# Kernel optimization log

Measured on AMD Instinct MI355X. Metric: run time of the kernel, lower is better.

## Reference

```python
import jax, jax.numpy as jnp
import numpy as np

B, N, D_IN, D_OUT = 4, 1024, 128, 64
SLOPE = 0.01  # LeakyReLU negative slope


def leaky_relu(x):
    return jnp.where(x >= 0, x, SLOPE * x)


def setup_inputs() -> dict:
    key = jax.random.key(0)
    k_x, k_m, k_w1, k_w2, k_a, k_l = jax.random.split(key, 6)
    x = jax.random.normal(k_x, (B, N, D_IN), dtype=jnp.float32)
    # binary adjacency mask; add self-loops so every row has >=1 neighbor
    mask = jax.random.bernoulli(k_m, 0.05, (B, N, N)).astype(jnp.float32)
    eye = jnp.eye(N, dtype=jnp.float32)[None]
    A_shape = jnp.maximum(mask, eye)
    w1 = jax.random.normal(k_w1, (D_IN, D_OUT), dtype=jnp.float32)
    w2 = jax.random.normal(k_w2, (D_IN, D_OUT), dtype=jnp.float32)
    a = jax.random.normal(k_a, (D_OUT,), dtype=jnp.float32)
    lin_w = jax.random.normal(k_l, (D_OUT, D_IN), dtype=jnp.float32) * (1.0 / np.sqrt(D_IN))
    return {"x": x, "A_shape": A_shape, "w1": w1, "w2": w2, "a": a, "lin_w": lin_w}


def reference(x, A_shape, w1, w2, a, lin_w):
    # x: [B,N,D_in], A_shape: [B,N,N] mask
    x1 = x @ w1            # [B,N,D_out]  (dst features)
    x2 = x @ w2            # [B,N,D_out]  (src features)
    # GATv2 additive score: leakyrelu(x1_i + x2_j) . a -> [B,N,N]
    S = leaky_relu(x1[:, :, None, :] + x2[:, None, :, :])
    S = jnp.einsum('bijd,d->bij', S, a)
    S = jnp.tanh(S / 8.0) * 8.0
    A = jnp.exp(S) * A_shape
    A = A / jnp.sum(A, axis=-1, keepdims=True)
    out = A @ x            # [B,N,D_in] weighted aggregate of raw features
    out = out @ lin_w.T    # [B,N,D_out]
    return leaky_relu(out)
```

## Files before the change

### kernel.cpp

```cpp
#include <hip/hip_runtime.h>
#include <math.h>

#define BB 4
#define NN 1024
#define DIN 128
#define DOUT 64
#define SLOPE 0.01f
#define RST 192
#define R1 8


__global__ __launch_bounds__(256, 2) void proj_kernel(
    const float* __restrict__ x, const float* __restrict__ w1,
    const float* __restrict__ w2, const float* __restrict__ lin_w,
    float* __restrict__ x12y) {
  int tid = threadIdx.x;
  int d = tid & 63;
  int g = tid >> 6;
  __shared__ __align__(16) float xl[R1][DIN];
  __shared__ float lwT[DIN][DOUT + 1];
  int row0 = blockIdx.x * R1;

  {
    const float4* xs = reinterpret_cast<const float4*>(x + (size_t)row0 * DIN);
    reinterpret_cast<float4*>(&xl[0][0])[tid] = xs[tid];
  }
#pragma unroll
  for (int i = 0; i < 32; ++i) {
    int idx = i * 256 + tid;
    lwT[idx & 127][idx >> 7] = lin_w[idx];
  }
  __syncthreads();

  float a1[2] = {0.f, 0.f};
  float a2[2] = {0.f, 0.f};
  float a3[2] = {0.f, 0.f};
  const float* w1c = w1 + d;
  const float* w2c = w2 + d;
#pragma unroll 4
  for (int k = 0; k < DIN; ++k) {
    float wv1 = w1c[k * DOUT];
    float wv2 = w2c[k * DOUT];
    float wv3 = lwT[k][d];
#pragma unroll
    for (int r = 0; r < 2; ++r) {
      float xv = xl[g * 2 + r][k];
      a1[r] = fmaf(xv, wv1, a1[r]);
      a2[r] = fmaf(xv, wv2, a2[r]);
      a3[r] = fmaf(xv, wv3, a3[r]);
    }
  }
#pragma unroll
  for (int r = 0; r < 2; ++r) {
    size_t o = (size_t)(row0 + g * 2 + r) * RST;
    x12y[o + d] = a1[r];
    x12y[o + DOUT + d] = a2[r];
    x12y[o + 2 * DOUT + d] = a3[r];
  }
}

__device__ __forceinline__ float fast_edge_exp(float sc) {
  float z = sc * 0.125f;
  z = fminf(10.f, fmaxf(-10.f, z));
  float u = __expf(2.f * z);
  float th = (u - 1.f) / (u + 1.f);
  return __expf(8.f * th);
}

__global__ __launch_bounds__(128, 8) void gat_row_kernel(
    const float* __restrict__ A_shape, const float* __restrict__ a_vec,
    const float* __restrict__ x12y, float* __restrict__ out) {
  int bi = blockIdx.x;
  int b = bi >> 10;
  int tid = threadIdx.x;
  int lane = tid & 63;
  int w = tid >> 6;

  __shared__ int eidx[1040];
  __shared__ __align__(16) float x1s[DOUT];
  __shared__ __align__(16) float avs[DOUT];
  __shared__ float aggh[2][DOUT];
  __shared__ float wsum[2];
  __shared__ int cnt[2];

  if (tid < DOUT) {
    x1s[tid] = x12y[(size_t)bi * RST + tid];
    avs[tid] = a_vec[tid];
  }

  const float* mask_row = A_shape + (size_t)bi * NN + w * 512;
  float mv[8];
#pragma unroll
  for (int c = 0; c < 8; ++c) mv[c] = mask_row[c * 64 + lane];
  int base = 0;
  int seg = w * 512;
#pragma unroll
  for (int c = 0; c < 8; ++c) {
    bool pred = (mv[c] != 0.f);
    unsigned long long m = __ballot(pred);
    int prefix = __popcll(m & ((1ull << lane) - 1ull));
    if (pred) eidx[seg + base + prefix] = w * 512 + c * 64 + lane;
    base += __popcll(m);
  }
  if (lane == 0) cnt[w] = base;
  __syncthreads();

  int nz0 = cnt[0], nz1 = cnt[1];
  int nzt = nz0 + nz1;
  int nzt8 = (nzt + 7) & ~7;
  if (tid < 8) {
    eidx[512 + nz1 + tid] = bi & (NN - 1);
  }
  __syncthreads();

  const float* x2b = x12y + (size_t)b * NN * RST + DOUT;
  const float* yb = x12y + (size_t)b * NN * RST + 2 * DOUT + lane;
  int l16 = tid & 15;
  int g0 = lane >> 4;
  float4 x1v = reinterpret_cast<const float4*>(x1s)[l16];
  float4 avv = reinterpret_cast<const float4*>(avs)[l16];
  float lsum = 0.f;
  float acc = 0.f;
  for (int s0 = 0; s0 < nzt8; s0 += 8) {
    int jj[4];
#pragma unroll
    for (int g2 = 0; g2 < 4; ++g2) {
      int ss = s0 + 4 * w + g2;
      int ps = (ss < nz0) ? ss : 512 + ss - nz0;
      jj[g2] = eidx[ps];
    }
    float yv[4];
#pragma unroll
    for (int g2 = 0; g2 < 4; ++g2) yv[g2] = yb[(size_t)jj[g2] * RST];
    float4 x2v = *reinterpret_cast<const float4*>(
        x2b + (size_t)jj[g0] * RST + l16 * 4);
    float z, sc = 0.f;
    z = x1v.x + x2v.x; sc = fmaf(z >= 0.f ? z : SLOPE * z, avv.x, sc);
    z = x1v.y + x2v.y; sc = fmaf(z >= 0.f ? z : SLOPE * z, avv.y, sc);
    z = x1v.z + x2v.z; sc = fmaf(z >= 0.f ? z : SLOPE * z, avv.z, sc);
    z = x1v.w + x2v.w; sc = fmaf(z >= 0.f ? z : SLOPE * z, avv.w, sc);
    sc += __shfl_xor(sc, 8, 16);
    sc += __shfl_xor(sc, 4, 16);
    sc += __shfl_xor(sc, 2, 16);
    sc += __shfl_xor(sc, 1, 16);
    float e = fast_edge_exp(sc);
    if (s0 + 4 * w + g0 >= nzt) e = 0.f;
    lsum += e;
#pragma unroll
    for (int g2 = 0; g2 < 4; ++g2) {
      float eg = __shfl(e, g2 * 16, 64);
      acc = fmaf(eg, yv[g2], acc);
    }
  }

#pragma unroll
  for (int off = 32; off > 0; off >>= 1) lsum += __shfl_xor(lsum, off, 64);
  if (lane == 0) wsum[w] = lsum;
  aggh[w][lane] = acc;
  __syncthreads();

  if (tid < DOUT) {
    float inv = 16.f / (wsum[0] + wsum[1]);
    float oo = (aggh[0][tid] + aggh[1][tid]) * inv;
    oo = oo >= 0.f ? oo : SLOPE * oo;
    out[(size_t)bi * DOUT + tid] = oo;
  }
}

extern "C" void kernel_launch(void* const* d_in, const int* in_sizes, int n_in,
                              void* d_out, int out_size, void* d_ws, size_t ws_size,
                              hipStream_t stream) {
  const float* x = (const float*)d_in[0];
  const float* A_shape = (const float*)d_in[1];
  const float* w1 = (const float*)d_in[2];
  const float* w2 = (const float*)d_in[3];
  const float* a = (const float*)d_in[4];
  const float* lin_w = (const float*)d_in[5];
  float* out = (float*)d_out;
  float* x12y = (float*)d_ws;

  proj_kernel<<<BB * NN / R1, 256, 0, stream>>>(x, w1, w2, lin_w, x12y);
  gat_row_kernel<<<BB * NN, 128, 0, stream>>>(A_shape, a, x12y, out);
}
```

Measured before the change: 99.18 us.

## Move mask compaction into projection kernel and use single-wave edge kernel

Mask-row compaction into 16-bit neighbor index lists now runs in extra blocks of the projection kernel, so it overlaps with the projection GEMM. The results are stored in the workspace together with per-row counts. The aggregation kernel becomes a single 64-lane wave per row that reads four packed indices per 64-bit load, with no LDS or block barriers. The trade-off is extra global traffic for the index lists and less per-row parallelism, since each row now gets one wave instead of two.

New measurement: 97.98 us. Within noise of the previous version (-1.2%).

```diff
diff --git a/kernel.cpp b/kernel.cpp
--- a/kernel.cpp
+++ b/kernel.cpp
@@ -8,13 +8,48 @@
 #define SLOPE 0.01f
 #define RST 192
 #define R1 8
+#define NPROJ (BB * NN / R1)
+#define NCOMP (BB * NN / 4)
+#define ESTRIDE 1056
 
 
-__global__ __launch_bounds__(256, 2) void proj_kernel(
+__device__ __forceinline__ float fast_edge_exp(float sc) {
+  float z = sc * 0.125f;
+  z = fminf(10.f, fmaxf(-10.f, z));
+  float u = __expf(2.f * z);
+  float th = (u - 1.f) / (u + 1.f);
+  return __expf(8.f * th);
+}
+
+__global__ __launch_bounds__(256, 2) void proj_compact_kernel(
     const float* __restrict__ x, const float* __restrict__ w1,
     const float* __restrict__ w2, const float* __restrict__ lin_w,
-    float* __restrict__ x12y) {
+    const float* __restrict__ A_shape, float* __restrict__ x12y,
+    int* __restrict__ cnt, unsigned short* __restrict__ ews) {
   int tid = threadIdx.x;
+
+  if (blockIdx.x >= NPROJ) {
+    int lane = tid & 63;
+    int r = (blockIdx.x - NPROJ) * 4 + (tid >> 6);
+    const float* mask_row = A_shape + (size_t)r * NN;
+    float mv[16];
+#pragma unroll
+    for (int c = 0; c < 16; ++c) mv[c] = mask_row[c * 64 + lane];
+    unsigned short* er = ews + (size_t)r * ESTRIDE;
+    int base = 0;
+#pragma unroll
+    for (int c = 0; c < 16; ++c) {
+      bool pred = (mv[c] != 0.f);
+      unsigned long long m = __ballot(pred);
+      int prefix = __popcll(m & ((1ull << lane) - 1ull));
+      if (pred) er[base + prefix] = (unsigned short)(c * 64 + lane);
+      base += __popcll(m);
+    }
+    if (lane < 4) er[base + lane] = (unsigned short)(r & (NN - 1));
+    if (lane == 0) cnt[r] = base;
+    return;
+  }
+
   int d = tid & 63;
   int g = tid >> 6;
   __shared__ __align__(16) float xl[R1][DIN];
@@ -59,81 +94,39 @@
   }
 }
 
-__device__ __forceinline__ float fast_edge_exp(float sc) {
-  float z = sc * 0.125f;
-  z = fminf(10.f, fmaxf(-10.f, z));
-  float u = __expf(2.f * z);
-  float th = (u - 1.f) / (u + 1.f);
-  return __expf(8.f * th);
-}
-
-__global__ __launch_bounds__(128, 8) void gat_row_kernel(
-    const float* __restrict__ A_shape, const float* __restrict__ a_vec,
-    const float* __restrict__ x12y, float* __restrict__ out) {
+__global__ __launch_bounds__(64, 8) void gat_edge_kernel(
+    const float* __restrict__ a_vec, const float* __restrict__ x12y,
+    const int* __restrict__ cnt, const unsigned short* __restrict__ ews,
+    float* __restrict__ out) {
   int bi = blockIdx.x;
   int b = bi >> 10;
-  int tid = threadIdx.x;
-  int lane = tid & 63;
-  int w = tid >> 6;
+  int lane = threadIdx.x;
+  int l16 = lane & 15;
+  int g0 = lane >> 4;
 
-  __shared__ int eidx[1040];
-  __shared__ __align__(16) float x1s[DOUT];
-  __shared__ __align__(16) float avs[DOUT];
-  __shared__ float aggh[2][DOUT];
-  __shared__ float wsum[2];
-  __shared__ int cnt[2];
-
-  if (tid < DOUT) {
-    x1s[tid] = x12y[(size_t)bi * RST + tid];
-    avs[tid] = a_vec[tid];
-  }
-
-  const float* mask_row = A_shape + (size_t)bi * NN + w * 512;
-  float mv[8];
-#pragma unroll
-  for (int c = 0; c < 8; ++c) mv[c] = mask_row[c * 64 + lane];
-  int base = 0;
-  int seg = w * 512;
-#pragma unroll
-  for (int c = 0; c < 8; ++c) {
-    bool pred = (mv[c] != 0.f);
-    unsigned long long m = __ballot(pred);
-    int prefix = __popcll(m & ((1ull << lane) - 1ull));
-    if (pred) eidx[seg + base + prefix] = w * 512 + c * 64 + lane;
-    base += __popcll(m);
-  }
-  if (lane == 0) cnt[w] = base;
-  __syncthreads();
-
-  int nz0 = cnt[0], nz1 = cnt[1];
-  int nzt = nz0 + nz1;
-  int nzt8 = (nzt + 7) & ~7;
-  if (tid < 8) {
-    eidx[512 + nz1 + tid] = bi & (NN - 1);
-  }
-  __syncthreads();
-
+  int nzt = cnt[bi];
+  int nzt4 = (nzt + 3) & ~3;
+  float4 x1v = reinterpret_cast<const float4*>(x12y + (size_t)bi * RST)[l16];
+  float4 avv = reinterpret_cast<const float4*>(a_vec)[l16];
   const float* x2b = x12y + (size_t)b * NN * RST + DOUT;
   const float* yb = x12y + (size_t)b * NN * RST + 2 * DOUT + lane;
-  int l16 = tid & 15;
-  int g0 = lane >> 4;
-  float4 x1v = reinterpret_cast<const float4*>(x1s)[l16];
-  float4 avv = reinterpret_cast<const float4*>(avs)[l16];
-  float lsum = 0.f;
-  float acc = 0.f;
-  for (int s0 = 0; s0 < nzt8; s0 += 8) {
-    int jj[4];
-#pragma unroll
-    for (int g2 = 0; g2 < 4; ++g2) {
-      int ss = s0 + 4 * w + g2;
-      int ps = (ss < nz0) ? ss : 512 + ss - nz0;
-      jj[g2] = eidx[ps];
-    }
-    float yv[4];
-#pragma unroll
-    for (int g2 = 0; g2 < 4; ++g2) yv[g2] = yb[(size_t)jj[g2] * RST];
+  const unsigned long long* e64 =
+      reinterpret_cast<const unsigned long long*>(ews + (size_t)bi * ESTRIDE);
+
+  float lsum = 0.f, acc = 0.f;
+  for (int s0 = 0; s0 < nzt4; s0 += 4) {
+    unsigned long long ej = e64[s0 >> 2];
+    int j0 = (int)(ej & 0xFFFFu);
+    int j1 = (int)((ej >> 16) & 0xFFFFu);
+    int j2 = (int)((ej >> 32) & 0xFFFFu);
+    int j3 = (int)(ej >> 48);
+    float yv0 = yb[(size_t)j0 * RST];
+    float yv1 = yb[(size_t)j1 * RST];
+    float yv2 = yb[(size_t)j2 * RST];
+    float yv3 = yb[(size_t)j3 * RST];
+    int jg = (g0 == 0) ? j0 : (g0 == 1) ? j1 : (g0 == 2) ? j2 : j3;
     float4 x2v = *reinterpret_cast<const float4*>(
-        x2b + (size_t)jj[g0] * RST + l16 * 4);
+        x2b + (size_t)jg * RST + l16 * 4);
     float z, sc = 0.f;
     z = x1v.x + x2v.x; sc = fmaf(z >= 0.f ? z : SLOPE * z, avv.x, sc);
     z = x1v.y + x2v.y; sc = fmaf(z >= 0.f ? z : SLOPE * z, avv.y, sc);
@@ -144,27 +137,19 @@
     sc += __shfl_xor(sc, 2, 16);
     sc += __shfl_xor(sc, 1, 16);
     float e = fast_edge_exp(sc);
-    if (s0 + 4 * w + g0 >= nzt) e = 0.f;
+    if (s0 + g0 >= nzt) e = 0.f;
     lsum += e;
-#pragma unroll
-    for (int g2 = 0; g2 < 4; ++g2) {
-      float eg = __shfl(e, g2 * 16, 64);
-      acc = fmaf(eg, yv[g2], acc);
-    }
+    acc = fmaf(__shfl(e, 0, 64), yv0, acc);
+    acc = fmaf(__shfl(e, 16, 64), yv1, acc);
+    acc = fmaf(__shfl(e, 32, 64), yv2, acc);
+    acc = fmaf(__shfl(e, 48, 64), yv3, acc);
   }
 
 #pragma unroll
   for (int off = 32; off > 0; off >>= 1) lsum += __shfl_xor(lsum, off, 64);
-  if (lane == 0) wsum[w] = lsum;
-  aggh[w][lane] = acc;
-  __syncthreads();
-
-  if (tid < DOUT) {
-    float inv = 16.f / (wsum[0] + wsum[1]);
-    float oo = (aggh[0][tid] + aggh[1][tid]) * inv;
-    oo = oo >= 0.f ? oo : SLOPE * oo;
-    out[(size_t)bi * DOUT + tid] = oo;
-  }
+  float oo = acc * (16.f / lsum);
+  oo = oo >= 0.f ? oo : SLOPE * oo;
+  out[(size_t)bi * DOUT + lane] = oo;
 }
 
 extern "C" void kernel_launch(void* const* d_in, const int* in_sizes, int n_in,
@@ -177,8 +162,12 @@
   const float* a = (const float*)d_in[4];
   const float* lin_w = (const float*)d_in[5];
   float* out = (float*)d_out;
-  float* x12y = (float*)d_ws;
+  char* ws = (char*)d_ws;
+  float* x12y = (float*)ws;
+  int* cnt = (int*)(ws + (size_t)BB * NN * RST * 4);
+  unsigned short* ews = (unsigned short*)(ws + (size_t)BB * NN * RST * 4 + BB * NN * 4);
 
-  proj_kernel<<<BB * NN / R1, 256, 0, stream>>>(x, w1, w2, lin_w, x12y);
-  gat_row_kernel<<<BB * NN, 128, 0, stream>>>(A_shape, a, x12y, out);
+  proj_compact_kernel<<<NPROJ + NCOMP, 256, 0, stream>>>(
+      x, w1, w2, lin_w, A_shape, x12y, cnt, ews);
+  gat_edge_kernel<<<BB * NN, 64, 0, stream>>>(a, x12y, cnt, ews, out);
 }
```
